# Performance work log

Measured on AMD Instinct MI355X. Metric: run time of the kernel, lower is better.

Reference implementation:

```python
import jax, jax.numpy as jnp
import numpy as np

N = 100000   # nodes
E = 1600000  # edges
H = 128      # num_features == hidden_size
C = 64       # num_classes
BN_EPS = 1e-5


def setup_inputs() -> dict:
    key = jax.random.key(0)
    ks = jax.random.split(key, 11)
    return {
        "x": jax.random.normal(ks[0], (N, H), jnp.float32),
        "edge_index": jax.random.randint(ks[1], (2, E), 0, N, dtype=jnp.int32),
        "edge_attr": jax.random.normal(ks[2], (E,), jnp.float32),
        "conv_w": jax.random.normal(ks[3], (2, 3, H, H), jnp.float32) / np.sqrt(H).astype(np.float32),
        "conv_b": jax.random.normal(ks[4], (2, 3, H), jnp.float32) * 0.1,
        "bn_g": jax.random.uniform(ks[5], (2, 3, H), jnp.float32, 0.5, 1.5),
        "bn_b": jax.random.normal(ks[6], (2, 3, H), jnp.float32) * 0.1,
        "bn_m": jax.random.normal(ks[7], (2, 3, H), jnp.float32) * 0.1,
        "bn_v": jax.random.uniform(ks[8], (2, 3, H), jnp.float32, 0.5, 1.5),
        "fc_w": jax.random.normal(ks[9], (H, C), jnp.float32) / np.sqrt(H).astype(np.float32),
        "fc_b": jax.random.normal(ks[10], (C,), jnp.float32) * 0.1,
    }


def _gin_conv(h, edge_index, w, b, g, beta, m, v):
    # GIN: out = MLP((1+eps)*x + sum_{j in N(i)} x_j), eps=0 (PyG default)
    src, dst = edge_index[0], edge_index[1]
    agg = jax.ops.segment_sum(h[src], dst, num_segments=N)  # [N,H] scatter-add
    h = h + agg
    for i in range(3):  # Linear -> BatchNorm1d (eval stats) -> ReLU
        h = h @ w[i] + b[i]
        h = (h - m[i]) * jax.lax.rsqrt(v[i] + BN_EPS) * g[i] + beta[i]
        h = jax.nn.relu(h)
    return h


def reference(x, edge_index, edge_attr, conv_w, conv_b, bn_g, bn_b, bn_m, bn_v, fc_w, fc_b):
    # edge_attr is ignored by default PyG GINConv (no edge weighting in GIN)
    h = jax.nn.relu(_gin_conv(x, edge_index, conv_w[0], conv_b[0], bn_g[0], bn_b[0], bn_m[0], bn_v[0]))
    h = jax.nn.relu(_gin_conv(h, edge_index, conv_w[1], conv_b[1], bn_g[1], bn_b[1], bn_m[1], bn_v[1]))
    # dropout is identity in eval mode
    logits = h @ fc_w + fc_b  # [N,C]
    return jax.nn.log_softmax(logits, axis=1)
```

## Files before the change

kernel.cpp:

```cpp
#include <hip/hip_runtime.h>

#define NN 100000
#define NE 1600000
#define HF 128
#define NC 64
#define AP 136
#define NB 196
#define BSH 9
#define BMASK 511
#define BCAP 9216

typedef __bf16 bf16x8 __attribute__((ext_vector_type(8)));
typedef float  f32x4  __attribute__((ext_vector_type(4)));
typedef unsigned short us8 __attribute__((ext_vector_type(8)));

__device__ __forceinline__ unsigned short f2b(float x) {
  unsigned int u = __float_as_uint(x);
  u += 0x7FFFu + ((u >> 16) & 1u);
  return (unsigned short)(u >> 16);
}
__device__ __forceinline__ float b2f(unsigned short b) {
  return __uint_as_float(((unsigned int)b) << 16);
}

__global__ void prep_weights(const float* __restrict__ conv_w, const float* __restrict__ conv_b,
                             const float* __restrict__ bn_g, const float* __restrict__ bn_b,
                             const float* __restrict__ bn_m, const float* __restrict__ bn_v,
                             const float* __restrict__ fc_w,
                             unsigned short* __restrict__ wt, unsigned short* __restrict__ wtf,
                             float* __restrict__ sarr, float* __restrict__ tarr) {
  int idx = blockIdx.x * 256 + threadIdx.x;
  if (idx < 6 * HF * HF) {
    int ls = idx / (HF * HF);
    int rem = idx - ls * HF * HF;
    int k = rem >> 7;
    int n = rem & 127;
    wt[(ls * HF + n) * HF + k] = f2b(conv_w[idx]);
  }
  if (idx < HF * NC) {
    int k = idx >> 6;
    int c = idx & 63;
    wtf[c * HF + k] = f2b(fc_w[idx]);
  }
  if (idx < 6 * HF) {
    float s = bn_g[idx] * rsqrtf(bn_v[idx] + 1e-5f);
    sarr[idx] = s;
    tarr[idx] = (conv_b[idx] - bn_m[idx]) * s + bn_b[idx];
  }
}

__global__ __launch_bounds__(256) void cast_bf16(const float* __restrict__ x,
                                                 unsigned short* __restrict__ xb) {
  size_t i = (size_t)(blockIdx.x * 256 + threadIdx.x) * 8;
  float4 a = *(const float4*)(x + i);
  float4 b = *(const float4*)(x + i + 4);
  us8 v = { f2b(a.x), f2b(a.y), f2b(a.z), f2b(a.w),
            f2b(b.x), f2b(b.y), f2b(b.z), f2b(b.w) };
  *(us8*)(xb + i) = v;
}

__global__ void init_gcur(int* __restrict__ gcur) {
  int t = threadIdx.x;
  if (t < NB) gcur[t] = t * BCAP;
}

__global__ __launch_bounds__(256) void bin_edges(const int* __restrict__ src,
                                                 const int* __restrict__ dst,
                                                 int* __restrict__ gcur,
                                                 unsigned int* __restrict__ binned) {
  __shared__ int hist[NB];
  int t = threadIdx.x;
  if (t < NB) hist[t] = 0;
  __syncthreads();
  int base = blockIdx.x * 8192;
  for (int j = 0; j < 32; j++) {
    int e = base + j * 256 + t;
    if (e < NE) atomicAdd(&hist[dst[e] >> BSH], 1);
  }
  __syncthreads();
  if (t < NB) {
    int c = hist[t];
    if (c) hist[t] = atomicAdd(&gcur[t], c);
  }
  __syncthreads();
  for (int j = 0; j < 32; j++) {
    int e = base + j * 256 + t;
    if (e < NE) {
      int d = dst[e];
      int b = d >> BSH;
      int p = atomicAdd(&hist[b], 1);
      binned[p] = (unsigned int)src[e] | ((unsigned int)(d & BMASK) << 17);
    }
  }
}

__global__ __launch_bounds__(256) void build_csr(const unsigned int* __restrict__ binned,
                                                 const int* __restrict__ gcur,
                                                 int* __restrict__ offs,
                                                 int* __restrict__ deg,
                                                 int* __restrict__ csr) {
  __shared__ int ncnt[512];
  __shared__ int sm[256];
  int t = threadIdx.x;
  int b = blockIdx.x;
  int beg = b * BCAP;
  int cntb = gcur[b] - beg;
  ncnt[t] = 0; ncnt[t + 256] = 0;
  __syncthreads();
  for (int e = beg + t; e < beg + cntb; e += 256) atomicAdd(&ncnt[binned[e] >> 17], 1);
  __syncthreads();
  int c0 = ncnt[2 * t], c1 = ncnt[2 * t + 1];
  int s = c0 + c1;
  sm[t] = s; __syncthreads();
  for (int off = 1; off < 256; off <<= 1) {
    int u = (t >= off) ? sm[t - off] : 0;
    __syncthreads();
    sm[t] += u;
    __syncthreads();
  }
  int ex = sm[t] - s + beg;
  int node0 = (b << BSH) + 2 * t;
  if (node0 < NN)     { offs[node0]     = ex;      deg[node0]     = c0; }
  if (node0 + 1 < NN) { offs[node0 + 1] = ex + c0; deg[node0 + 1] = c1; }
  ncnt[2 * t]     = ex;
  ncnt[2 * t + 1] = ex + c0;
  __syncthreads();
  for (int e = beg + t; e < beg + cntb; e += 256) {
    unsigned int u = binned[e];
    int p = atomicAdd(&ncnt[u >> 17], 1);
    csr[p] = (int)(u & 0x1FFFFu);
  }
}

__global__ __launch_bounds__(256) void aggregate(const unsigned short* __restrict__ h,
                                                 const int* __restrict__ offs,
                                                 const int* __restrict__ deg,
                                                 const int* __restrict__ csr,
                                                 unsigned short* __restrict__ out) {
  int wave = threadIdx.x >> 6;
  int lane = threadIdx.x & 63;
  int node = blockIdx.x * 4 + wave;
  if (node >= NN) return;
  int g  = lane >> 4;
  int sl = lane & 15;
  int beg = offs[node];
  int dg  = deg[node];

  float acc[8];
  if (g == 0) {
    us8 v = *(const us8*)(h + (size_t)node * HF + sl * 8);
    #pragma unroll
    for (int i = 0; i < 8; i++) acc[i] = b2f(v[i]);
  } else {
    #pragma unroll
    for (int i = 0; i < 8; i++) acc[i] = 0.f;
  }

  for (int e = beg + g; e < beg + dg; e += 4) {
    int s = csr[e];
    us8 v = *(const us8*)(h + (size_t)s * HF + sl * 8);
    #pragma unroll
    for (int i = 0; i < 8; i++) acc[i] += b2f(v[i]);
  }

  #pragma unroll
  for (int i = 0; i < 8; i++) {
    acc[i] += __shfl_xor(acc[i], 16, 64);
    acc[i] += __shfl_xor(acc[i], 32, 64);
  }
  if (g == 0) {
    us8 r;
    #pragma unroll
    for (int i = 0; i < 8; i++) r[i] = f2b(acc[i]);
    *(us8*)(out + (size_t)node * HF + sl * 8) = r;
  }
}

__device__ __forceinline__ void stage_tile(const unsigned short* __restrict__ in,
                                           unsigned short* Ab, int row0, int t) {
  for (int it = 0; it < 4; it++) {
    int idx = it * 256 + t;
    int r = idx >> 4;
    int c = (idx & 15) << 3;
    int gr = row0 + r;
    us8 v = (us8)(0);
    if (gr < NN) v = *(const us8*)(in + (size_t)gr * HF + c);
    *(us8*)&Ab[r * AP + c] = v;
  }
}

__device__ __forceinline__ void mlp3_tile(unsigned short* Ab, unsigned short* Wb,
                                          const unsigned short* __restrict__ wt,
                                          const float* __restrict__ sarr,
                                          const float* __restrict__ tarr,
                                          int layer, int t, int wave, int lane) {
  int m = lane & 15, q = lane >> 4;
  const unsigned short* wbase = wt + layer * 3 * HF * HF;
  for (int sub = 0; sub < 3; sub++) {
    __syncthreads();
    const unsigned short* wsub = wbase + sub * HF * HF;
    for (int it = 0; it < 8; it++) {
      int idx = it * 256 + t;
      int r = idx >> 4;
      int c = (idx & 15) << 3;
      *(us8*)&Wb[r * AP + c] = *(const us8*)(wsub + r * HF + c);
    }
    __syncthreads();

    bf16x8 af[4];
    #pragma unroll
    for (int k0 = 0; k0 < 4; k0++)
      af[k0] = *(const bf16x8*)&Ab[(wave * 16 + m) * AP + k0 * 32 + q * 8];

    f32x4 acc[8];
    #pragma unroll
    for (int nt = 0; nt < 8; nt++) {
      acc[nt] = (f32x4){0.f, 0.f, 0.f, 0.f};
      #pragma unroll
      for (int k0 = 0; k0 < 4; k0++) {
        bf16x8 bf = *(const bf16x8*)&Wb[(nt * 16 + m) * AP + k0 * 32 + q * 8];
        acc[nt] = __builtin_amdgcn_mfma_f32_16x16x32_bf16(af[k0], bf, acc[nt], 0, 0, 0);
      }
    }

    const float* sp = sarr + (layer * 3 + sub) * HF;
    const float* tp = tarr + (layer * 3 + sub) * HF;
    #pragma unroll
    for (int nt = 0; nt < 8; nt++) {
      int c = nt * 16 + m;
      float sc = sp[c], sh = tp[c];
      #pragma unroll
      for (int i = 0; i < 4; i++) {
        int r = wave * 16 + q * 4 + i;
        float y = fmaxf(acc[nt][i] * sc + sh, 0.f);
        Ab[r * AP + c] = f2b(y);
      }
    }
  }
}

__global__ __launch_bounds__(256) void mlp3(const unsigned short* __restrict__ in,
                                            unsigned short* __restrict__ out,
                                            const unsigned short* __restrict__ wt,
                                            const float* __restrict__ sarr,
                                            const float* __restrict__ tarr) {
  __shared__ unsigned short Ab[64 * AP];
  __shared__ unsigned short Wb[HF * AP];
  int t = threadIdx.x;
  int lane = t & 63, wave = t >> 6;
  int row0 = blockIdx.x * 64;

  stage_tile(in, Ab, row0, t);
  mlp3_tile(Ab, Wb, wt, sarr, tarr, 0, t, wave, lane);

  __syncthreads();
  for (int it = 0; it < 4; it++) {
    int idx = it * 256 + t;
    int r = idx >> 4;
    int c = (idx & 15) << 3;
    int gr = row0 + r;
    if (gr < NN) *(us8*)(out + (size_t)gr * HF + c) = *(const us8*)&Ab[r * AP + c];
  }
}

__global__ __launch_bounds__(256) void mlp3fc(const unsigned short* __restrict__ in,
                                              float* __restrict__ out,
                                              const unsigned short* __restrict__ wt,
                                              const float* __restrict__ sarr,
                                              const float* __restrict__ tarr,
                                              const unsigned short* __restrict__ wtf,
                                              const float* __restrict__ fc_b) {
  __shared__ unsigned short Ab[64 * AP];
  __shared__ unsigned short Wb[HF * AP];
  int t = threadIdx.x;
  int lane = t & 63, wave = t >> 6;
  int row0 = blockIdx.x * 64;

  stage_tile(in, Ab, row0, t);
  mlp3_tile(Ab, Wb, wt, sarr, tarr, 1, t, wave, lane);

  __syncthreads();
  for (int it = 0; it < 4; it++) {
    int idx = it * 256 + t;
    int r = idx >> 4;
    int c = (idx & 15) << 3;
    *(us8*)&Wb[r * AP + c] = *(const us8*)(wtf + r * HF + c);
  }
  __syncthreads();

  int m = lane & 15, q = lane >> 4;
  bf16x8 af[4];
  #pragma unroll
  for (int k0 = 0; k0 < 4; k0++)
    af[k0] = *(const bf16x8*)&Ab[(wave * 16 + m) * AP + k0 * 32 + q * 8];

  f32x4 acc[4];
  #pragma unroll
  for (int nt = 0; nt < 4; nt++) {
    acc[nt] = (f32x4){0.f, 0.f, 0.f, 0.f};
    #pragma unroll
    for (int k0 = 0; k0 < 4; k0++) {
      bf16x8 bf = *(const bf16x8*)&Wb[(nt * 16 + m) * AP + k0 * 32 + q * 8];
      acc[nt] = __builtin_amdgcn_mfma_f32_16x16x32_bf16(af[k0], bf, acc[nt], 0, 0, 0);
    }
  }
  float v[4][4];
  #pragma unroll
  for (int nt = 0; nt < 4; nt++) {
    float b = fc_b[nt * 16 + m];
    #pragma unroll
    for (int i = 0; i < 4; i++) v[nt][i] = acc[nt][i] + b;
  }
  float mx[4], sum[4];
  #pragma unroll
  for (int i = 0; i < 4; i++) {
    mx[i] = fmaxf(fmaxf(v[0][i], v[1][i]), fmaxf(v[2][i], v[3][i]));
    mx[i] = fmaxf(mx[i], __shfl_xor(mx[i], 1, 64));
    mx[i] = fmaxf(mx[i], __shfl_xor(mx[i], 2, 64));
    mx[i] = fmaxf(mx[i], __shfl_xor(mx[i], 4, 64));
    mx[i] = fmaxf(mx[i], __shfl_xor(mx[i], 8, 64));
    sum[i] = __expf(v[0][i] - mx[i]) + __expf(v[1][i] - mx[i])
           + __expf(v[2][i] - mx[i]) + __expf(v[3][i] - mx[i]);
    sum[i] += __shfl_xor(sum[i], 1, 64);
    sum[i] += __shfl_xor(sum[i], 2, 64);
    sum[i] += __shfl_xor(sum[i], 4, 64);
    sum[i] += __shfl_xor(sum[i], 8, 64);
    sum[i] = __logf(sum[i]) + mx[i];
  }
  #pragma unroll
  for (int i = 0; i < 4; i++) {
    int gr = row0 + wave * 16 + q * 4 + i;
    if (gr < NN) {
      #pragma unroll
      for (int nt = 0; nt < 4; nt++)
        out[(size_t)gr * NC + nt * 16 + m] = v[nt][i] - sum[i];
    }
  }
}

extern "C" void kernel_launch(void* const* d_in, const int* in_sizes, int n_in,
                              void* d_out, int out_size, void* d_ws, size_t ws_size,
                              hipStream_t stream) {
  const float* x      = (const float*)d_in[0];
  const int*   ei     = (const int*)d_in[1];
  const float* conv_w = (const float*)d_in[3];
  const float* conv_b = (const float*)d_in[4];
  const float* bn_g   = (const float*)d_in[5];
  const float* bn_b   = (const float*)d_in[6];
  const float* bn_m   = (const float*)d_in[7];
  const float* bn_v   = (const float*)d_in[8];
  const float* fc_w   = (const float*)d_in[9];
  const float* fc_b   = (const float*)d_in[10];
  float* out = (float*)d_out;

  const int* srcI = ei;
  const int* dstI = ei + NE;

  unsigned short* Xb   = (unsigned short*)d_ws;
  unsigned short* Abuf = Xb + (size_t)NN * HF;
  unsigned short* Bbuf = Abuf + (size_t)NN * HF;
  int* gcur   = (int*)(Bbuf + (size_t)NN * HF);
  int* offs   = gcur + 256;
  int* deg    = offs + 100004;
  unsigned int* binned = (unsigned int*)(deg + 100004);
  int* csr    = (int*)(binned + (size_t)NB * BCAP);
  unsigned short* wt  = (unsigned short*)(csr + (size_t)NB * BCAP);
  unsigned short* wtf = wt + 6 * HF * HF;
  float* sarr = (float*)(wtf + HF * NC);
  float* tarr = sarr + 6 * HF;

  prep_weights<<<384, 256, 0, stream>>>(conv_w, conv_b, bn_g, bn_b, bn_m, bn_v, fc_w,
                                        wt, wtf, sarr, tarr);
  cast_bf16<<<6250, 256, 0, stream>>>(x, Xb);
  init_gcur<<<1, 256, 0, stream>>>(gcur);
  bin_edges<<<196, 256, 0, stream>>>(srcI, dstI, gcur, binned);
  build_csr<<<196, 256, 0, stream>>>(binned, gcur, offs, deg, csr);

  aggregate<<<NN / 4, 256, 0, stream>>>(Xb, offs, deg, csr, Abuf);
  mlp3<<<(NN + 63) / 64, 256, 0, stream>>>(Abuf, Bbuf, wt, sarr, tarr);
  aggregate<<<NN / 4, 256, 0, stream>>>(Bbuf, offs, deg, csr, Abuf);
  mlp3fc<<<(NN + 63) / 64, 256, 0, stream>>>(Abuf, out, wt, sarr, tarr, wtf, fc_b);
}
```

Before: 384.5 us.

## Pre-swizzle weights into MFMA fragment order and load B operands directly from global

```diff
diff --git a/kernel.cpp b/kernel.cpp
--- a/kernel.cpp
+++ b/kernel.cpp
@@ -31,16 +31,25 @@
                              float* __restrict__ sarr, float* __restrict__ tarr) {
   int idx = blockIdx.x * 256 + threadIdx.x;
   if (idx < 6 * HF * HF) {
-    int ls = idx / (HF * HF);
-    int rem = idx - ls * HF * HF;
-    int k = rem >> 7;
-    int n = rem & 127;
-    wt[(ls * HF + n) * HF + k] = f2b(conv_w[idx]);
+    int j  = idx & 7;
+    int m  = (idx >> 3) & 15;
+    int q  = (idx >> 7) & 3;
+    int nt = (idx >> 9) & 7;
+    int k0 = (idx >> 12) & 3;
+    int ls = idx >> 14;
+    int k = k0 * 32 + q * 8 + j;
+    int n = nt * 16 + m;
+    wt[idx] = f2b(conv_w[(ls * HF + k) * HF + n]);
   }
   if (idx < HF * NC) {
-    int k = idx >> 6;
-    int c = idx & 63;
-    wtf[c * HF + k] = f2b(fc_w[idx]);
+    int j  = idx & 7;
+    int m  = (idx >> 3) & 15;
+    int q  = (idx >> 7) & 3;
+    int nt = (idx >> 9) & 3;
+    int k0 = idx >> 11;
+    int k = k0 * 32 + q * 8 + j;
+    int c = nt * 16 + m;
+    wtf[idx] = f2b(fc_w[k * NC + c]);
   }
   if (idx < 6 * HF) {
     float s = bn_g[idx] * rsqrtf(bn_v[idx] + 1e-5f);
@@ -176,53 +185,34 @@
   }
 }
 
-__device__ __forceinline__ void stage_tile(const unsigned short* __restrict__ in,
-                                           unsigned short* Ab, int row0, int t) {
-  for (int it = 0; it < 4; it++) {
-    int idx = it * 256 + t;
-    int r = idx >> 4;
-    int c = (idx & 15) << 3;
-    int gr = row0 + r;
-    us8 v = (us8)(0);
-    if (gr < NN) v = *(const us8*)(in + (size_t)gr * HF + c);
-    *(us8*)&Ab[r * AP + c] = v;
-  }
-}
-
-__device__ __forceinline__ void mlp3_tile(unsigned short* Ab, unsigned short* Wb,
+__device__ __forceinline__ void mlp3_body(const unsigned short* __restrict__ in,
+                                          unsigned short* Ab,
                                           const unsigned short* __restrict__ wt,
                                           const float* __restrict__ sarr,
                                           const float* __restrict__ tarr,
-                                          int layer, int t, int wave, int lane) {
+                                          int layer, int row0, int wave, int lane,
+                                          bf16x8 af[4]) {
   int m = lane & 15, q = lane >> 4;
-  const unsigned short* wbase = wt + layer * 3 * HF * HF;
+  int node = row0 + wave * 16 + m;
+  int nclamp = (node < NN) ? node : 0;
+  #pragma unroll
+  for (int k0 = 0; k0 < 4; k0++)
+    af[k0] = *(const bf16x8*)(in + (size_t)nclamp * HF + k0 * 32 + q * 8);
+
+  const unsigned short* wbase = wt + layer * 3 * 16384;
+  #pragma unroll
   for (int sub = 0; sub < 3; sub++) {
-    __syncthreads();
-    const unsigned short* wsub = wbase + sub * HF * HF;
-    for (int it = 0; it < 8; it++) {
-      int idx = it * 256 + t;
-      int r = idx >> 4;
-      int c = (idx & 15) << 3;
-      *(us8*)&Wb[r * AP + c] = *(const us8*)(wsub + r * HF + c);
-    }
-    __syncthreads();
-
-    bf16x8 af[4];
-    #pragma unroll
-    for (int k0 = 0; k0 < 4; k0++)
-      af[k0] = *(const bf16x8*)&Ab[(wave * 16 + m) * AP + k0 * 32 + q * 8];
-
+    const unsigned short* wsub = wbase + sub * 16384;
     f32x4 acc[8];
     #pragma unroll
     for (int nt = 0; nt < 8; nt++) {
       acc[nt] = (f32x4){0.f, 0.f, 0.f, 0.f};
       #pragma unroll
       for (int k0 = 0; k0 < 4; k0++) {
-        bf16x8 bf = *(const bf16x8*)&Wb[(nt * 16 + m) * AP + k0 * 32 + q * 8];
+        bf16x8 bf = *(const bf16x8*)(wsub + ((k0 * 8 + nt) * 64 + lane) * 8);
         acc[nt] = __builtin_amdgcn_mfma_f32_16x16x32_bf16(af[k0], bf, acc[nt], 0, 0, 0);
       }
     }
-
     const float* sp = sarr + (layer * 3 + sub) * HF;
     const float* tp = tarr + (layer * 3 + sub) * HF;
     #pragma unroll
@@ -236,6 +226,9 @@
         Ab[r * AP + c] = f2b(y);
       }
     }
+    #pragma unroll
+    for (int k0 = 0; k0 < 4; k0++)
+      af[k0] = *(const bf16x8*)&Ab[(wave * 16 + m) * AP + k0 * 32 + q * 8];
   }
 }
 
@@ -245,18 +238,15 @@
                                             const float* __restrict__ sarr,
                                             const float* __restrict__ tarr) {
   __shared__ unsigned short Ab[64 * AP];
-  __shared__ unsigned short Wb[HF * AP];
   int t = threadIdx.x;
   int lane = t & 63, wave = t >> 6;
   int row0 = blockIdx.x * 64;
-
-  stage_tile(in, Ab, row0, t);
-  mlp3_tile(Ab, Wb, wt, sarr, tarr, 0, t, wave, lane);
-
-  __syncthreads();
+  bf16x8 af[4];
+  mlp3_body(in, Ab, wt, sarr, tarr, 0, row0, wave, lane, af);
+
   for (int it = 0; it < 4; it++) {
-    int idx = it * 256 + t;
-    int r = idx >> 4;
+    int idx = it * 64 + lane;
+    int r = wave * 16 + (idx >> 4);
     int c = (idx & 15) << 3;
     int gr = row0 + r;
     if (gr < NN) *(us8*)(out + (size_t)gr * HF + c) = *(const us8*)&Ab[r * AP + c];
@@ -271,28 +261,12 @@
                                               const unsigned short* __restrict__ wtf,
                                               const float* __restrict__ fc_b) {
   __shared__ unsigned short Ab[64 * AP];
-  __shared__ unsigned short Wb[HF * AP];
   int t = threadIdx.x;
   int lane = t & 63, wave = t >> 6;
   int row0 = blockIdx.x * 64;
-
-  stage_tile(in, Ab, row0, t);
-  mlp3_tile(Ab, Wb, wt, sarr, tarr, 1, t, wave, lane);
-
-  __syncthreads();
-  for (int it = 0; it < 4; it++) {
-    int idx = it * 256 + t;
-    int r = idx >> 4;
-    int c = (idx & 15) << 3;
-    *(us8*)&Wb[r * AP + c] = *(const us8*)(wtf + r * HF + c);
-  }
-  __syncthreads();
-
   int m = lane & 15, q = lane >> 4;
   bf16x8 af[4];
-  #pragma unroll
-  for (int k0 = 0; k0 < 4; k0++)
-    af[k0] = *(const bf16x8*)&Ab[(wave * 16 + m) * AP + k0 * 32 + q * 8];
+  mlp3_body(in, Ab, wt, sarr, tarr, 1, row0, wave, lane, af);
 
   f32x4 acc[4];
   #pragma unroll
@@ -300,7 +274,7 @@
     acc[nt] = (f32x4){0.f, 0.f, 0.f, 0.f};
     #pragma unroll
     for (int k0 = 0; k0 < 4; k0++) {
-      bf16x8 bf = *(const bf16x8*)&Wb[(nt * 16 + m) * AP + k0 * 32 + q * 8];
+      bf16x8 bf = *(const bf16x8*)(wtf + ((k0 * 4 + nt) * 64 + lane) * 8);
       acc[nt] = __builtin_amdgcn_mfma_f32_16x16x32_bf16(af[k0], bf, acc[nt], 0, 0, 0);
     }
   }
```

Result: no change. 383.3 us (-0.3%).
